# Kernel tuning notes

Measured on AMD Instinct MI355X. Metric: run time of the kernel, lower is better.

The kernel has to match this reference:

```python
import jax, jax.numpy as jnp
import numpy as np

BATCH, C_IN, H = 16, 32, 224
N_FILT, K = 64, 5


def setup_inputs() -> dict:
    key = jax.random.key(0)
    k1, k2 = jax.random.split(key)
    x = jax.random.normal(k1, (BATCH, C_IN, H, H), dtype=jnp.float32)
    weight = jax.random.normal(k2, (N_FILT, C_IN, K, K), dtype=jnp.float32)
    bias = jnp.zeros((N_FILT,), dtype=jnp.float32)  # torch init: zeros(1) per filter
    return {"x": x, "weight": weight, "bias": bias}


def reference(x, weight, bias):
    # Fully-connected conv layer: stride 1, VALID padding.
    # Equivalent to stacking per-filter sum(x_patch * w) + scalar bias.
    out = jax.lax.conv_general_dilated(
        x, weight,
        window_strides=(1, 1),
        padding='VALID',
        dimension_numbers=('NCHW', 'OIHW', 'NCHW'),
    )
    # per-filter scalar bias broadcast over spatial dims
    return out + bias[None, :, None, None]
```

## Files before the change

### kernel.cpp

```cpp
#include <hip/hip_runtime.h>

#define CI    32
#define IH    224
#define IW    224
#define OHS   220
#define OWS   220
#define NF    64
#define KS    5
#define XCOLS 228
#define CP    36
#define WPD   40
#define XROWS 8
#define NBUFW (KS * NF * WPD)

typedef __attribute__((ext_vector_type(4))) float   f32x4;
typedef __attribute__((ext_vector_type(4))) __bf16  bf16x4;
typedef __attribute__((ext_vector_type(8))) __bf16  bf16x8;

__global__ void repack_w_kernel(const float* __restrict__ w, __bf16* __restrict__ wp) {
  int i = blockIdx.x * 256 + threadIdx.x;
  if (i >= KS * KS * NF * CI) return;
  int c   = i & (CI - 1);
  int f   = (i >> 5) & (NF - 1);
  int tap = i >> 11;
  int kh = tap / KS, kw = tap % KS;
  wp[i] = (__bf16)w[((f * CI + c) * KS + kh) * KS + kw];
}

template <bool USE_WS>
__global__ __launch_bounds__(512, 1)
void conv_main(const float* __restrict__ x, const float* __restrict__ w,
               const __bf16* __restrict__ wp, const float* __restrict__ bias,
               float* __restrict__ out) {
  __shared__ __bf16 xs[XROWS * XCOLS * CP];
  __shared__ __bf16 wsm[NBUFW];

  const int tid  = threadIdx.x;
  const int lane = tid & 63;
  const int wv   = tid >> 6;
  const int m    = lane & 15;
  const int q    = lane >> 4;

  int bid = blockIdx.x;
  int lid = (bid >> 3) + (bid & 7) * 110;
  const int n   = lid / 55;
  const int oh0 = (lid % 55) * 4;

  {
    const float* xn = x + (size_t)n * CI * IH * IW;
    for (int p = tid; p < XROWS * 56 * 8; p += 512) {
      int pc   = p & 7;
      int pg   = p >> 3;
      int pcol = pg % 56;
      int prow = pg / 56;
      int row  = oh0 + prow;
      f32x4 v0 = *(const f32x4*)(xn + ((size_t)(pc * 4 + 0) * IH + row) * IW + pcol * 4);
      f32x4 v1 = *(const f32x4*)(xn + ((size_t)(pc * 4 + 1) * IH + row) * IW + pcol * 4);
      f32x4 v2 = *(const f32x4*)(xn + ((size_t)(pc * 4 + 2) * IH + row) * IW + pcol * 4);
      f32x4 v3 = *(const f32x4*)(xn + ((size_t)(pc * 4 + 3) * IH + row) * IW + pcol * 4);
#pragma unroll
      for (int dcol = 0; dcol < 4; ++dcol) {
        bf16x4 t;
        t[0] = (__bf16)v0[dcol]; t[1] = (__bf16)v1[dcol];
        t[2] = (__bf16)v2[dcol]; t[3] = (__bf16)v3[dcol];
        *(bf16x4*)&xs[(prow * XCOLS + pcol * 4 + dcol) * CP + pc * 4] = t;
      }
    }
    for (int z = tid; z < XROWS * 4 * CP; z += 512) {
      int rr  = z / (4 * CP);
      int rem = z - rr * (4 * CP);
      xs[(rr * XCOLS + 224) * CP + rem] = (__bf16)0.0f;
    }
  }

  if (USE_WS) {
    for (int i = tid; i < NF * CI * KS / 8; i += 512) {
      int c0 = (i & 3) * 8;
      int f  = (i >> 2) & 63;
      int kw = i >> 8;
      bf16x8 v = *(const bf16x8*)(wp + ((size_t)(0 * KS + kw) * NF + f) * CI + c0);
      *(bf16x8*)&wsm[(kw * NF + f) * WPD + c0] = v;
    }
  } else {
    for (int i = tid; i < KS * NF * CI; i += 512) {
      int c  = i & 31;
      int f  = (i >> 5) & 63;
      int kw = i >> 11;
      wsm[(kw * NF + f) * WPD + c] = (__bf16)w[((f * CI + c) * KS + 0) * KS + kw];
    }
  }
  __syncthreads();

  int rj[7], cbj[7], xoff[7];
#pragma unroll
  for (int j = 0; j < 7; ++j) {
    int t   = wv + j * 8;
    rj[j]   = t / 14;
    cbj[j]  = (t % 14) * 16;
    xoff[j] = (rj[j] * XCOLS + cbj[j] + m) * CP + q * 8;
  }

  f32x4 acc[28];
#pragma unroll
  for (int i = 0; i < 28; ++i) { f32x4 z = {0.f, 0.f, 0.f, 0.f}; acc[i] = z; }

  for (int kh = 0; kh < KS; ++kh) {
    bf16x8 pw[3];
    if (USE_WS && kh < KS - 1) {
#pragma unroll
      for (int it = 0; it < 3; ++it) {
        int e = it * 512 + tid;
        if (e < 1280) {
          int c0 = (e & 3) * 8;
          int f  = (e >> 2) & 63;
          int kw = e >> 8;
          pw[it] = *(const bf16x8*)(wp + ((size_t)((kh + 1) * KS + kw) * NF + f) * CI + c0);
        }
      }
    }

#pragma unroll
    for (int kw = 0; kw < KS; ++kw) {
      bf16x8 af[4];
#pragma unroll
      for (int ft = 0; ft < 4; ++ft)
        af[ft] = *(const bf16x8*)&wsm[(kw * NF + ft * 16 + m) * WPD + q * 8];
#pragma unroll
      for (int j = 0; j < 7; ++j) {
        const __bf16* bp = &xs[xoff[j] + (kh * XCOLS + kw) * CP];
        bf16x4 lo = *(const bf16x4*)bp;
        bf16x4 hi = *(const bf16x4*)(bp + 4);
        bf16x8 bv8 = __builtin_shufflevector(lo, hi, 0, 1, 2, 3, 4, 5, 6, 7);
#pragma unroll
        for (int ft = 0; ft < 4; ++ft)
          acc[j * 4 + ft] =
              __builtin_amdgcn_mfma_f32_16x16x32_bf16(af[ft], bv8, acc[j * 4 + ft], 0, 0, 0);
      }
    }

    if (kh < KS - 1) {
      __syncthreads();
      if (USE_WS) {
#pragma unroll
        for (int it = 0; it < 3; ++it) {
          int e = it * 512 + tid;
          if (e < 1280) {
            int c0 = (e & 3) * 8;
            int f  = (e >> 2) & 63;
            int kw = e >> 8;
            *(bf16x8*)&wsm[(kw * NF + f) * WPD + c0] = pw[it];
          }
        }
      } else {
        for (int i = tid; i < KS * NF * CI; i += 512) {
          int c  = i & 31;
          int f  = (i >> 5) & 63;
          int kw = i >> 11;
          wsm[(kw * NF + f) * WPD + c] =
              (__bf16)w[((f * CI + c) * KS + (kh + 1)) * KS + kw];
        }
      }
      __syncthreads();
    }
  }

  float bvv[16];
#pragma unroll
  for (int ft = 0; ft < 4; ++ft)
#pragma unroll
    for (int rg = 0; rg < 4; ++rg)
      bvv[ft * 4 + rg] = bias[ft * 16 + q * 4 + rg];

#pragma unroll
  for (int j = 0; j < 7; ++j) {
    int ow = cbj[j] + m;
    if (ow < OWS) {
      int oh = oh0 + rj[j];
#pragma unroll
      for (int ft = 0; ft < 4; ++ft) {
#pragma unroll
        for (int rg = 0; rg < 4; ++rg) {
          int f = ft * 16 + q * 4 + rg;
          out[(((size_t)n * NF + f) * OHS + oh) * OWS + ow] = acc[j * 4 + ft][rg] + bvv[ft * 4 + rg];
        }
      }
    }
  }
}

extern "C" void kernel_launch(void* const* d_in, const int* in_sizes, int n_in,
                              void* d_out, int out_size, void* d_ws, size_t ws_size,
                              hipStream_t stream) {
  const float* x    = (const float*)d_in[0];
  const float* w    = (const float*)d_in[1];
  const float* bias = (const float*)d_in[2];
  float* out = (float*)d_out;

  const int NW = KS * KS * NF * CI;
  if (ws_size >= (size_t)NW * sizeof(__bf16)) {
    __bf16* wp = (__bf16*)d_ws;
    repack_w_kernel<<<(NW + 255) / 256, 256, 0, stream>>>(w, wp);
    conv_main<true><<<880, 512, 0, stream>>>(x, w, wp, bias, out);
  } else {
    conv_main<false><<<880, 512, 0, stream>>>(x, w, nullptr, bias, out);
  }
}
```

Before: 374.0 us.

## Pre-transform input to NHWC bf16 and add direct-load conv kernel

Adds a separate pass that converts the fp32 NCHW input into a bf16 NHWC tensor in workspace. A new conv kernel then reads MFMA B-operands straight from global/L2 with 16-byte loads instead of staging input tiles in LDS. It uses smaller 256-thread blocks with higher occupancy, and each wave computes half an output row. This removes the in-kernel transpose/convert and the large LDS tile, but adds an extra global write and read of about 51MB. It also reloads weights into LDS per kh without double buffering.

After: 503.4 us. +34.6%, slower.

```diff
diff --git a/kernel.cpp b/kernel.cpp
--- a/kernel.cpp
+++ b/kernel.cpp
@@ -27,6 +27,100 @@
   wp[i] = (__bf16)w[((f * CI + c) * KS + kh) * KS + kw];
 }
 
+__global__ __launch_bounds__(256)
+void x_transform(const float* __restrict__ x, __bf16* __restrict__ xh) {
+  int chunk = blockIdx.x * 256 + threadIdx.x;
+  int c8  = (chunk & 3) * 8;
+  int pos = chunk >> 2;
+  int w   = pos % IW;
+  int nh  = pos / IW;
+  int n   = nh / IH;
+  int h   = nh - n * IH;
+  const float* xp = x + ((size_t)n * CI + c8) * (IH * IW) + h * IW + w;
+  bf16x8 v;
+#pragma unroll
+  for (int j = 0; j < 8; ++j) v[j] = (__bf16)xp[(size_t)j * (IH * IW)];
+  *(bf16x8*)(xh + (size_t)pos * CI + c8) = v;
+}
+
+__global__ __launch_bounds__(256, 3)
+void conv_direct(const __bf16* __restrict__ xh, const __bf16* __restrict__ wp,
+                 const float* __restrict__ bias, float* __restrict__ out) {
+  __shared__ __bf16 wsm[KS * NF * WPD];
+
+  const int tid  = threadIdx.x;
+  const int lane = tid & 63;
+  const int wv   = tid >> 6;
+  const int m    = lane & 15;
+  const int q    = lane >> 4;
+
+  const int bid  = blockIdx.x;
+  const int lid  = (bid & 7) * 220 + (bid >> 3);
+  const int task = lid * 4 + wv;
+  const int n    = task / 440;
+  const int r    = task - n * 440;
+  const int oh   = r >> 1;
+  const int ow0  = (r & 1) * 112;
+
+  const __bf16* xb = xh + (((size_t)n * IH + oh) * IW + ow0 + m) * CI + q * 8;
+
+  f32x4 acc[28];
+#pragma unroll
+  for (int i = 0; i < 28; ++i) { f32x4 z = {0.f, 0.f, 0.f, 0.f}; acc[i] = z; }
+
+  for (int kh = 0; kh < KS; ++kh) {
+    if (kh) __syncthreads();
+#pragma unroll
+    for (int it = 0; it < 5; ++it) {
+      int i  = it * 256 + tid;
+      int c0 = (i & 3) * 8;
+      int f  = (i >> 2) & 63;
+      int kw = i >> 8;
+      *(bf16x8*)&wsm[(kw * NF + f) * WPD + c0] =
+          *(const bf16x8*)(wp + (((size_t)kh * KS + kw) * NF + f) * CI + c0);
+    }
+    __syncthreads();
+
+    const __bf16* xr = xb + (size_t)kh * (IW * CI);
+#pragma unroll
+    for (int kw = 0; kw < KS; ++kw) {
+      bf16x8 af[4];
+#pragma unroll
+      for (int ft = 0; ft < 4; ++ft)
+        af[ft] = *(const bf16x8*)&wsm[(kw * NF + ft * 16 + m) * WPD + q * 8];
+#pragma unroll
+      for (int j = 0; j < 7; ++j) {
+        bf16x8 bv = *(const bf16x8*)(xr + (j * 16 + kw) * CI);
+#pragma unroll
+        for (int ft = 0; ft < 4; ++ft)
+          acc[j * 4 + ft] =
+              __builtin_amdgcn_mfma_f32_16x16x32_bf16(af[ft], bv, acc[j * 4 + ft], 0, 0, 0);
+      }
+    }
+  }
+
+  float bvv[16];
+#pragma unroll
+  for (int ft = 0; ft < 4; ++ft)
+#pragma unroll
+    for (int rg = 0; rg < 4; ++rg)
+      bvv[ft * 4 + rg] = bias[ft * 16 + q * 4 + rg];
+
+#pragma unroll
+  for (int j = 0; j < 7; ++j) {
+    int ow = ow0 + j * 16 + m;
+    if (ow < OWS) {
+#pragma unroll
+      for (int ft = 0; ft < 4; ++ft)
+#pragma unroll
+        for (int rg = 0; rg < 4; ++rg) {
+          int f = ft * 16 + q * 4 + rg;
+          out[(((size_t)n * NF + f) * OHS + oh) * OWS + ow] = acc[j * 4 + ft][rg] + bvv[ft * 4 + rg];
+        }
+    }
+  }
+}
+
 template <bool USE_WS>
 __global__ __launch_bounds__(512, 1)
 void conv_main(const float* __restrict__ x, const float* __restrict__ w,
@@ -196,8 +290,17 @@
   const float* bias = (const float*)d_in[2];
   float* out = (float*)d_out;
 
-  const int NW = KS * KS * NF * CI;
-  if (ws_size >= (size_t)NW * sizeof(__bf16)) {
+  const int    NW = KS * KS * NF * CI;
+  const size_t WB = (size_t)NW * sizeof(__bf16);
+  const size_t XB = (size_t)16 * IH * IW * CI * sizeof(__bf16);
+
+  if (ws_size >= WB + XB + 256) {
+    __bf16* wp  = (__bf16*)d_ws;
+    __bf16* xhp = (__bf16*)((char*)d_ws + WB);
+    repack_w_kernel<<<(NW + 255) / 256, 256, 0, stream>>>(w, wp);
+    x_transform<<<(16 * IH * IW * 4) / 256, 256, 0, stream>>>(x, xhp);
+    conv_direct<<<1760, 256, 0, stream>>>(xhp, wp, bias, out);
+  } else if (ws_size >= WB) {
     __bf16* wp = (__bf16*)d_ws;
     repack_w_kernel<<<(NW + 255) / 256, 256, 0, stream>>>(w, wp);
     conv_main<true><<<880, 512, 0, stream>>>(x, w, wp, bias, out);
```
